# Performance work log

Hardware: AMD Instinct MI355X
Metric: run time of the kernel (lower is better)

## Reference

```python
import jax, jax.numpy as jnp
import numpy as np

D_MODEL = 64
NUM_HEADS = 4
HEAD_DIM = D_MODEL // NUM_HEADS  # 16
SEQ_LEN = 8192


def setup_inputs() -> dict:
    key = jax.random.key(0)
    kx, kq, kk, kv, kbq, kbk, kbv = jax.random.split(key, 7)
    bound = 1.0 / np.sqrt(D_MODEL)  # torch nn.Linear default init range
    x = jax.random.normal(kx, (SEQ_LEN, D_MODEL), dtype=jnp.float32)
    Wq = jax.random.uniform(kq, (HEAD_DIM, D_MODEL), minval=-bound, maxval=bound, dtype=jnp.float32)
    Wk = jax.random.uniform(kk, (HEAD_DIM, D_MODEL), minval=-bound, maxval=bound, dtype=jnp.float32)
    Wv = jax.random.uniform(kv, (HEAD_DIM, D_MODEL), minval=-bound, maxval=bound, dtype=jnp.float32)
    bq = jax.random.uniform(kbq, (HEAD_DIM,), minval=-bound, maxval=bound, dtype=jnp.float32)
    bk = jax.random.uniform(kbk, (HEAD_DIM,), minval=-bound, maxval=bound, dtype=jnp.float32)
    bv = jax.random.uniform(kbv, (HEAD_DIM,), minval=-bound, maxval=bound, dtype=jnp.float32)
    return {"x": x, "Wq": Wq, "bq": bq, "Wk": Wk, "bk": bk, "Wv": Wv, "bv": bv}


def reference(x, Wq, bq, Wk, bk, Wv, bv):
    # Linear projections (torch nn.Linear: x @ W.T + b)
    Q = x @ Wq.T + bq  # [S, HEAD_DIM]
    K = x @ Wk.T + bk  # [S, HEAD_DIM]
    V = x @ Wv.T + bv  # [S, HEAD_DIM]
    scale = 1.0 / np.sqrt(HEAD_DIM).astype(np.float32)
    scores = (Q @ K.T) * scale  # [S, S]
    # causal mask: triu(ones, diagonal=1) positions set to -inf
    s = scores.shape[-1]
    causal = jnp.tril(jnp.ones((s, s), dtype=bool))  # True = keep
    scores = jnp.where(causal, scores, -jnp.inf)
    attn = jax.nn.softmax(scores, axis=-1)
    return attn @ V  # [S, HEAD_DIM]
```

## Files before the change

kernel.cpp:

```cpp
#include <hip/hip_runtime.h>
#include <hip/hip_fp16.h>

#define SEQ 8192
#define CHUNK 32
#define NST 256
#define TOTAL_CHUNKS 2176
#define NQT 512

typedef __fp16   fp16x2 __attribute__((ext_vector_type(2)));
typedef __fp16   fp16x4 __attribute__((ext_vector_type(4)));
typedef _Float16 half4  __attribute__((ext_vector_type(4)));
typedef _Float16 half8  __attribute__((ext_vector_type(8)));
typedef float   floatx4 __attribute__((ext_vector_type(4)));

__device__ __forceinline__ int cum_chunks(int n) {
    const int a = n >> 4, r = n & 15;
    return (a + 1) * (8 * a + r);
}

__device__ __forceinline__ half4 pk4(float a, float b, float c, float d) {
    const fp16x2 lo = __builtin_amdgcn_cvt_pkrtz(a, b);
    const fp16x2 hi = __builtin_amdgcn_cvt_pkrtz(c, d);
    const fp16x4 v  = __builtin_shufflevector(lo, hi, 0, 1, 2, 3);
    return __builtin_bit_cast(half4, v);
}

__global__ __launch_bounds__(256) void proj_kernel(
    const float* __restrict__ x,
    const float* __restrict__ Wq, const float* __restrict__ bq,
    const float* __restrict__ Wk, const float* __restrict__ bk,
    const float* __restrict__ Wv, const float* __restrict__ bv,
    _Float16* __restrict__ Q, _Float16* __restrict__ KV)
{
    __shared__ float4 xs[16][17];
    __shared__ float4 wqs[16][17];
    __shared__ float4 wks[16][17];
    __shared__ float4 wvs[16][17];

    const int tid  = threadIdx.x;
    const int r    = tid >> 4;
    const int d    = tid & 15;
    const int row0 = blockIdx.x * 16;

    const int rr  = tid >> 4;
    const int cc4 = tid & 15;
    xs[rr][cc4]  = *(const float4*)(x  + (size_t)row0 * 64 + tid * 4);
    wqs[rr][cc4] = *(const float4*)(Wq + tid * 4);
    wks[rr][cc4] = *(const float4*)(Wk + tid * 4);
    wvs[rr][cc4] = *(const float4*)(Wv + tid * 4);
    __syncthreads();

    float aq = 0.f, ak = 0.f, av = 0.f;
#pragma unroll
    for (int kk = 0; kk < 16; ++kk) {
        const float4 xv = xs[r][kk];
        const float4 q4 = wqs[d][kk];
        const float4 k4 = wks[d][kk];
        const float4 v4 = wvs[d][kk];
        aq += xv.x * q4.x; aq += xv.y * q4.y; aq += xv.z * q4.z; aq += xv.w * q4.w;
        ak += xv.x * k4.x; ak += xv.y * k4.y; ak += xv.z * k4.z; ak += xv.w * k4.w;
        av += xv.x * v4.x; av += xv.y * v4.y; av += xv.z * v4.z; av += xv.w * v4.w;
    }
    aq += bq[d];
    ak += bk[d];
    av += bv[d];
    aq *= 0.36067376022224085f;

    const int row = row0 + r;
    Q[row * 16 + d] = (_Float16)aq;
    _Float16* kvb = KV + (size_t)blockIdx.x * 512;
    kvb[((d >> 2) * 16 + r) * 8 + (d & 3)]     = (_Float16)ak;
    kvb[((r >> 2) * 16 + d) * 8 + 4 + (r & 3)] = (_Float16)av;
}

__global__ __launch_bounds__(64) void flash_kernel(
    const _Float16* __restrict__ Q, const _Float16* __restrict__ KV,
    float* __restrict__ partO, float* __restrict__ partL)
{
    const int bp = (TOTAL_CHUNKS - 1) - (int)blockIdx.x;
    int lo = 0, hi = NST - 1;
#pragma unroll
    for (int it = 0; it < 8; ++it) {
        const int mid = (lo + hi + 1) >> 1;
        if (cum_chunks(mid) <= bp) lo = mid; else hi = mid - 1;
    }
    const int st = lo;
    const int c  = bp - cum_chunks(st);
    const int t0 = c * CHUNK;
    const int nk = 2 * st + 2;
    int t1 = t0 + CHUNK;
    if (t1 > nk) t1 = nk;
    const int td0 = 2 * st;
    const int nd  = (t1 < td0) ? t1 : td0;

    const int L    = threadIdx.x;
    const int m16  = L & 15;
    const int quad = L >> 4;
    const int qrA  = st * 32 + m16;
    const int qrB  = qrA + 16;

    const half4 qfA = *(const half4*)(Q + (size_t)qrA * 16 + quad * 4);
    const half4 qfB = *(const half4*)(Q + (size_t)qrB * 16 + quad * 4);
    const _Float16* kvbase = KV + (size_t)L * 8;

    const floatx4 z4 = {0.f, 0.f, 0.f, 0.f};

    auto ldkv = [&](int t) -> half8 {
        return *(const half8*)(kvbase + (size_t)t * 512);
    };

    float   lA = 0.f, lB = 0.f;
    floatx4 accA = {0.f, 0.f, 0.f, 0.f};
    floatx4 accB = {0.f, 0.f, 0.f, 0.f};

    auto body2 = [&](half8 kv) {
        const half4 kf = __builtin_shufflevector(kv, kv, 0, 1, 2, 3);
        const half4 vf = __builtin_shufflevector(kv, kv, 4, 5, 6, 7);
        floatx4 sA = __builtin_amdgcn_mfma_f32_16x16x16f16(kf, qfA, z4, 0, 0, 0);
        floatx4 sB = __builtin_amdgcn_mfma_f32_16x16x16f16(kf, qfB, z4, 0, 0, 0);
        const float a0 = __builtin_amdgcn_exp2f(sA[0]);
        const float a1 = __builtin_amdgcn_exp2f(sA[1]);
        const float a2 = __builtin_amdgcn_exp2f(sA[2]);
        const float a3 = __builtin_amdgcn_exp2f(sA[3]);
        const float b0 = __builtin_amdgcn_exp2f(sB[0]);
        const float b1 = __builtin_amdgcn_exp2f(sB[1]);
        const float b2 = __builtin_amdgcn_exp2f(sB[2]);
        const float b3 = __builtin_amdgcn_exp2f(sB[3]);
        lA += (a0 + a1) + (a2 + a3);
        lB += (b0 + b1) + (b2 + b3);
        const half4 pA = pk4(a0, a1, a2, a3);
        const half4 pB = pk4(b0, b1, b2, b3);
        accA = __builtin_amdgcn_mfma_f32_16x16x16f16(vf, pA, accA, 0, 0, 0);
        accB = __builtin_amdgcn_mfma_f32_16x16x16f16(vf, pB, accB, 0, 0, 0);
    };

    int kt = t0;
    if (kt + 1 < nd) {
        half8 v0 = ldkv(kt);
        half8 v1 = ldkv(kt + 1);
        for (; kt + 3 < nd; kt += 2) {
            const half8 n0 = ldkv(kt + 2);
            const half8 n1 = ldkv(kt + 3);
            __builtin_amdgcn_s_setprio(1);
            body2(v0);
            body2(v1);
            __builtin_amdgcn_s_setprio(0);
            v0 = n0; v1 = n1;
        }
        body2(v0);
        body2(v1);
        kt += 2;
    }

    if (t1 == nk) {
        {
            const half8 kv = ldkv(td0);
            const half4 kf = __builtin_shufflevector(kv, kv, 0, 1, 2, 3);
            const half4 vf = __builtin_shufflevector(kv, kv, 4, 5, 6, 7);
            floatx4 sA = __builtin_amdgcn_mfma_f32_16x16x16f16(kf, qfA, z4, 0, 0, 0);
#pragma unroll
            for (int r = 0; r < 4; ++r)
                if (quad * 4 + r > m16) sA[r] = -1.0e30f;
            floatx4 sB = __builtin_amdgcn_mfma_f32_16x16x16f16(kf, qfB, z4, 0, 0, 0);
            const float a0 = __builtin_amdgcn_exp2f(sA[0]);
            const float a1 = __builtin_amdgcn_exp2f(sA[1]);
            const float a2 = __builtin_amdgcn_exp2f(sA[2]);
            const float a3 = __builtin_amdgcn_exp2f(sA[3]);
            const float b0 = __builtin_amdgcn_exp2f(sB[0]);
            const float b1 = __builtin_amdgcn_exp2f(sB[1]);
            const float b2 = __builtin_amdgcn_exp2f(sB[2]);
            const float b3 = __builtin_amdgcn_exp2f(sB[3]);
            lA += (a0 + a1) + (a2 + a3);
            lB += (b0 + b1) + (b2 + b3);
            const half4 pA = pk4(a0, a1, a2, a3);
            const half4 pB = pk4(b0, b1, b2, b3);
            accA = __builtin_amdgcn_mfma_f32_16x16x16f16(vf, pA, accA, 0, 0, 0);
            accB = __builtin_amdgcn_mfma_f32_16x16x16f16(vf, pB, accB, 0, 0, 0);
        }
        {
            const half8 kv = ldkv(td0 + 1);
            const half4 kf = __builtin_shufflevector(kv, kv, 0, 1, 2, 3);
            const half4 vf = __builtin_shufflevector(kv, kv, 4, 5, 6, 7);
            floatx4 sB = __builtin_amdgcn_mfma_f32_16x16x16f16(kf, qfB, z4, 0, 0, 0);
#pragma unroll
            for (int r = 0; r < 4; ++r)
                if (quad * 4 + r > m16) sB[r] = -1.0e30f;
            const float b0 = __builtin_amdgcn_exp2f(sB[0]);
            const float b1 = __builtin_amdgcn_exp2f(sB[1]);
            const float b2 = __builtin_amdgcn_exp2f(sB[2]);
            const float b3 = __builtin_amdgcn_exp2f(sB[3]);
            lB += (b0 + b1) + (b2 + b3);
            const half4 pB = pk4(b0, b1, b2, b3);
            accB = __builtin_amdgcn_mfma_f32_16x16x16f16(vf, pB, accB, 0, 0, 0);
        }
    }

    lA += __shfl_xor(lA, 16);
    lA += __shfl_xor(lA, 32);
    lB += __shfl_xor(lB, 16);
    lB += __shfl_xor(lB, 32);

    float* po = partO + (size_t)bp * 512;
    *(floatx4*)(po + m16 * 16 + quad * 4)       = accA;
    *(floatx4*)(po + 256 + m16 * 16 + quad * 4) = accB;
    if (quad == 0) {
        partL[(size_t)bp * 32 + m16]      = lA;
        partL[(size_t)bp * 32 + 16 + m16] = lB;
    }
}

__global__ __launch_bounds__(256) void merge_kernel(
    const float* __restrict__ partO, const float* __restrict__ partL,
    float* __restrict__ out)
{
    const int qt = blockIdx.x;
    const int t  = threadIdx.x;
    const int st = qt >> 1;
    const int hf = qt & 1;

    const int base = cum_chunks(st);
    const int nc   = (st >> 4) + 1;

    const float* po = partO + (size_t)base * 512 + hf * 256 + t;
    const float* pl = partL + (size_t)base * 32 + hf * 16 + (t >> 4);
    float Ls = 0.f, O = 0.f;
    for (int c = 0; c < nc; ++c, po += 512, pl += 32) {
        O  += *po;
        Ls += *pl;
    }
    out[(size_t)qt * 256 + t] = O / Ls;
}

extern "C" void kernel_launch(void* const* d_in, const int* in_sizes, int n_in,
                              void* d_out, int out_size, void* d_ws, size_t ws_size,
                              hipStream_t stream) {
    const float* x  = (const float*)d_in[0];
    const float* Wq = (const float*)d_in[1];
    const float* bq = (const float*)d_in[2];
    const float* Wk = (const float*)d_in[3];
    const float* bk = (const float*)d_in[4];
    const float* Wv = (const float*)d_in[5];
    const float* bv = (const float*)d_in[6];

    char* ws = (char*)d_ws;
    _Float16* Q     = (_Float16*)(ws);
    _Float16* KV    = (_Float16*)(ws + 262144);
    float*    partO = (float*)(ws + 786432);
    float*    partL = (float*)(ws + 786432 + 4456448);

    proj_kernel<<<dim3(SEQ / 16), dim3(256), 0, stream>>>(
        x, Wq, bq, Wk, bk, Wv, bv, Q, KV);
    flash_kernel<<<dim3(TOTAL_CHUNKS), dim3(64), 0, stream>>>(
        Q, KV, partO, partL);
    merge_kernel<<<dim3(NQT), dim3(256), 0, stream>>>(
        partO, partL, (float*)d_out);
}
```

Before: 84.91 us.

## Split flash chunk key tiles across two wavefronts and reduce via LDS

Each flash block now has two wavefronts. They take alternating key tiles of the chunk, and each handles one of the two diagonal tiles. Their partial O and l accumulators are summed through shared memory before wave 0 writes the partials. This halves the serial per-block dependency chain and doubles the waves available for latency hiding, at the cost of a __syncthreads and an LDS reduction. The packed rtz fp16 conversion is also replaced with plain casts, which changes the rounding mode and may emit different instructions.

```diff
diff --git a/kernel.cpp b/kernel.cpp
--- a/kernel.cpp
+++ b/kernel.cpp
@@ -7,8 +7,6 @@
 #define TOTAL_CHUNKS 2176
 #define NQT 512
 
-typedef __fp16   fp16x2 __attribute__((ext_vector_type(2)));
-typedef __fp16   fp16x4 __attribute__((ext_vector_type(4)));
 typedef _Float16 half4  __attribute__((ext_vector_type(4)));
 typedef _Float16 half8  __attribute__((ext_vector_type(8)));
 typedef float   floatx4 __attribute__((ext_vector_type(4)));
@@ -16,13 +14,6 @@
 __device__ __forceinline__ int cum_chunks(int n) {
     const int a = n >> 4, r = n & 15;
     return (a + 1) * (8 * a + r);
-}
-
-__device__ __forceinline__ half4 pk4(float a, float b, float c, float d) {
-    const fp16x2 lo = __builtin_amdgcn_cvt_pkrtz(a, b);
-    const fp16x2 hi = __builtin_amdgcn_cvt_pkrtz(c, d);
-    const fp16x4 v  = __builtin_shufflevector(lo, hi, 0, 1, 2, 3);
-    return __builtin_bit_cast(half4, v);
 }
 
 __global__ __launch_bounds__(256) void proj_kernel(
@@ -73,7 +64,7 @@
     kvb[((r >> 2) * 16 + d) * 8 + 4 + (r & 3)] = (_Float16)av;
 }
 
-__global__ __launch_bounds__(64) void flash_kernel(
+__global__ __launch_bounds__(128) void flash_kernel(
     const _Float16* __restrict__ Q, const _Float16* __restrict__ KV,
     float* __restrict__ partO, float* __restrict__ partL)
 {
@@ -93,7 +84,9 @@
     const int td0 = 2 * st;
     const int nd  = (t1 < td0) ? t1 : td0;
 
-    const int L    = threadIdx.x;
+    const int tid  = threadIdx.x;
+    const int w    = tid >> 6;
+    const int L    = tid & 63;
     const int m16  = L & 15;
     const int quad = L >> 4;
     const int qrA  = st * 32 + m16;
@@ -128,19 +121,19 @@
         const float b3 = __builtin_amdgcn_exp2f(sB[3]);
         lA += (a0 + a1) + (a2 + a3);
         lB += (b0 + b1) + (b2 + b3);
-        const half4 pA = pk4(a0, a1, a2, a3);
-        const half4 pB = pk4(b0, b1, b2, b3);
+        const half4 pA = {(_Float16)a0, (_Float16)a1, (_Float16)a2, (_Float16)a3};
+        const half4 pB = {(_Float16)b0, (_Float16)b1, (_Float16)b2, (_Float16)b3};
         accA = __builtin_amdgcn_mfma_f32_16x16x16f16(vf, pA, accA, 0, 0, 0);
         accB = __builtin_amdgcn_mfma_f32_16x16x16f16(vf, pB, accB, 0, 0, 0);
     };
 
-    int kt = t0;
-    if (kt + 1 < nd) {
+    int kt = t0 + w;
+    if (kt + 2 < nd) {
         half8 v0 = ldkv(kt);
-        half8 v1 = ldkv(kt + 1);
-        for (; kt + 3 < nd; kt += 2) {
-            const half8 n0 = ldkv(kt + 2);
-            const half8 n1 = ldkv(kt + 3);
+        half8 v1 = ldkv(kt + 2);
+        for (; kt + 6 < nd; kt += 4) {
+            const half8 n0 = ldkv(kt + 4);
+            const half8 n1 = ldkv(kt + 6);
             __builtin_amdgcn_s_setprio(1);
             body2(v0);
             body2(v1);
@@ -149,11 +142,13 @@
         }
         body2(v0);
         body2(v1);
-        kt += 2;
-    }
+        kt += 4;
+    }
+    if (kt < nd)
+        body2(ldkv(kt));
 
     if (t1 == nk) {
-        {
+        if (w == 0) {
             const half8 kv = ldkv(td0);
             const half4 kf = __builtin_shufflevector(kv, kv, 0, 1, 2, 3);
             const half4 vf = __builtin_shufflevector(kv, kv, 4, 5, 6, 7);
@@ -172,12 +167,11 @@
             const float b3 = __builtin_amdgcn_exp2f(sB[3]);
             lA += (a0 + a1) + (a2 + a3);
             lB += (b0 + b1) + (b2 + b3);
-            const half4 pA = pk4(a0, a1, a2, a3);
-            const half4 pB = pk4(b0, b1, b2, b3);
+            const half4 pA = {(_Float16)a0, (_Float16)a1, (_Float16)a2, (_Float16)a3};
+            const half4 pB = {(_Float16)b0, (_Float16)b1, (_Float16)b2, (_Float16)b3};
             accA = __builtin_amdgcn_mfma_f32_16x16x16f16(vf, pA, accA, 0, 0, 0);
             accB = __builtin_amdgcn_mfma_f32_16x16x16f16(vf, pB, accB, 0, 0, 0);
-        }
-        {
+        } else {
             const half8 kv = ldkv(td0 + 1);
             const half4 kf = __builtin_shufflevector(kv, kv, 0, 1, 2, 3);
             const half4 vf = __builtin_shufflevector(kv, kv, 4, 5, 6, 7);
@@ -190,7 +184,7 @@
             const float b2 = __builtin_amdgcn_exp2f(sB[2]);
             const float b3 = __builtin_amdgcn_exp2f(sB[3]);
             lB += (b0 + b1) + (b2 + b3);
-            const half4 pB = pk4(b0, b1, b2, b3);
+            const half4 pB = {(_Float16)b0, (_Float16)b1, (_Float16)b2, (_Float16)b3};
             accB = __builtin_amdgcn_mfma_f32_16x16x16f16(vf, pB, accB, 0, 0, 0);
         }
     }
@@ -200,12 +194,31 @@
     lB += __shfl_xor(lB, 16);
     lB += __shfl_xor(lB, 32);
 
-    float* po = partO + (size_t)bp * 512;
-    *(floatx4*)(po + m16 * 16 + quad * 4)       = accA;
-    *(floatx4*)(po + 256 + m16 * 16 + quad * 4) = accB;
-    if (quad == 0) {
-        partL[(size_t)bp * 32 + m16]      = lA;
-        partL[(size_t)bp * 32 + 16 + m16] = lB;
+    __shared__ floatx4 sOA[64];
+    __shared__ floatx4 sOB[64];
+    __shared__ float   sLA[16];
+    __shared__ float   sLB[16];
+    if (w == 1) {
+        sOA[L] = accA;
+        sOB[L] = accB;
+        if (quad == 0) { sLA[m16] = lA; sLB[m16] = lB; }
+    }
+    __syncthreads();
+    if (w == 0) {
+        const floatx4 oa = sOA[L];
+        const floatx4 ob = sOB[L];
+        accA[0] += oa[0]; accA[1] += oa[1]; accA[2] += oa[2]; accA[3] += oa[3];
+        accB[0] += ob[0]; accB[1] += ob[1]; accB[2] += ob[2]; accB[3] += ob[3];
+        lA += sLA[m16];
+        lB += sLB[m16];
+
+        float* po = partO + (size_t)bp * 512;
+        *(floatx4*)(po + m16 * 16 + quad * 4)       = accA;
+        *(floatx4*)(po + 256 + m16 * 16 + quad * 4) = accB;
+        if (quad == 0) {
+            partL[(size_t)bp * 32 + m16]      = lA;
+            partL[(size_t)bp * 32 + 16 + m16] = lB;
+        }
     }
 }
 
@@ -250,7 +263,7 @@
 
     proj_kernel<<<dim3(SEQ / 16), dim3(256), 0, stream>>>(
         x, Wq, bq, Wk, bk, Wv, bv, Q, KV);
-    flash_kernel<<<dim3(TOTAL_CHUNKS), dim3(64), 0, stream>>>(
+    flash_kernel<<<dim3(TOTAL_CHUNKS), dim3(128), 0, stream>>>(
         Q, KV, partO, partL);
     merge_kernel<<<dim3(NQT), dim3(256), 0, stream>>>(
         partO, partL, (float*)d_out);
```

New measurement: 84.27 us. No clear change (-0.8%).
